# Kernel tuning notes

Measured on AMD Instinct MI355X. Metric: run time of the kernel, lower is better.

Reference implementation:

```python
import jax, jax.numpy as jnp
import numpy as np

N_TOKEN = 8192
N_EMBED = 512
N_SAMPLE = 10
TAU = 1.0
RHO = 1.0


def setup_inputs() -> dict:
    key = jax.random.key(0)
    k1, k2 = jax.random.split(key)
    inputs = jax.random.normal(k1, (4, 2048, N_EMBED), dtype=jnp.float32)
    embeds = jax.random.normal(k2, (N_TOKEN, N_EMBED), dtype=jnp.float32)
    return {"inputs": inputs, "embeds": embeds}


def reference(inputs, embeds):
    size = inputs.shape
    x = inputs.reshape(-1, N_EMBED)  # (N, D)
    n = x.shape[0]
    # squared distances, scaled by n_token (as in get_distances)
    dists = (jnp.sum(x * x, axis=-1, keepdims=True)
             + jnp.sum(embeds * embeds, axis=-1)[None, :]
             - 2.0 * jnp.matmul(x, embeds.T)) / N_TOKEN  # (N, K)
    logits = -dists / TAU  # categorical(softmax(logits)) == categorical(logits)
    skey = jax.random.fold_in(jax.random.key(0), 1)
    # multinomial with replacement: n_sample i.i.d. categorical draws per row
    samples = jax.random.categorical(skey, logits[:, None, :], axis=-1,
                                     shape=(n, N_SAMPLE))  # (N, n_sample) int
    quantized_embs = embeds[samples].mean(axis=1)  # (N, D) gather + mean
    quantized = x + jax.lax.stop_gradient(quantized_embs - x)  # straight-through
    gkey = jax.random.fold_in(jax.random.key(0), 2)
    gates = jax.random.bernoulli(gkey, RHO, (n,)).astype(x.dtype)[:, None]
    quantized = quantized * gates + (1.0 - gates) * x
    quantized = quantized.reshape(size)
    samples = samples.reshape(size[:-1] + (N_SAMPLE,))
    return quantized, samples
```

## Files before the change

### kernel.cpp

```cpp
#include <hip/hip_runtime.h>
#include <stdint.h>
#include <math.h>

#define N_ROWS 8192
#define N_TOK  8192
#define N_DIM  512
#define N_SAMP 10
#define GK     1536

typedef __attribute__((ext_vector_type(8))) short bf16x8_t;
typedef __attribute__((ext_vector_type(4))) float f32x4_t;

__host__ __device__ __forceinline__ void tf2x32(uint32_t ks0, uint32_t ks1,
                                                uint32_t& x0, uint32_t& x1) {
  uint32_t ks2 = ks0 ^ ks1 ^ 0x1BD11BDAu;
  x0 += ks0; x1 += ks1;
#define TF_ROUND(r) { x0 += x1; x1 = (x1 << (r)) | (x1 >> (32 - (r))); x1 ^= x0; }
  TF_ROUND(13) TF_ROUND(15) TF_ROUND(26) TF_ROUND(6)
  x0 += ks1; x1 += ks2 + 1u;
  TF_ROUND(17) TF_ROUND(29) TF_ROUND(16) TF_ROUND(24)
  x0 += ks2; x1 += ks0 + 2u;
  TF_ROUND(13) TF_ROUND(15) TF_ROUND(26) TF_ROUND(6)
  x0 += ks0; x1 += ks1 + 3u;
  TF_ROUND(17) TF_ROUND(29) TF_ROUND(16) TF_ROUND(24)
  x0 += ks1; x1 += ks2 + 4u;
  TF_ROUND(13) TF_ROUND(15) TF_ROUND(26) TF_ROUND(6)
  x0 += ks2; x1 += ks0 + 5u;
#undef TF_ROUND
}

__device__ __forceinline__ unsigned short f2bf_rne(float f) {
  uint32_t u = __float_as_uint(f);
  uint32_t r = (u + 0x7fffu + ((u >> 16) & 1u)) >> 16;
  return (unsigned short)r;
}
__device__ __forceinline__ float bf2f(unsigned short h) {
  return __uint_as_float((uint32_t)h << 16);
}

__device__ __forceinline__ unsigned long long shfl_xor_u64(unsigned long long v, int off) {
  uint32_t lo = (uint32_t)v, hi = (uint32_t)(v >> 32);
  lo = (uint32_t)__shfl_xor((int)lo, off, 64);
  hi = (uint32_t)__shfl_xor((int)hi, off, 64);
  return ((unsigned long long)hi << 32) | lo;
}

__global__ __launch_bounds__(256) void rownorm_kernel(const float* __restrict__ M,
                                                      float* __restrict__ out) {
  int lane = threadIdx.x & 63;
  int row = (int)((blockIdx.x * blockDim.x + threadIdx.x) >> 6);
  const float* p = M + (size_t)row * N_DIM;
  float acc = 0.f;
#pragma unroll
  for (int d = 0; d < N_DIM; d += 64) {
    float v = p[d + lane];
    acc = fmaf(v, v, acc);
  }
#pragma unroll
  for (int off = 32; off; off >>= 1) acc += __shfl_xor(acc, off, 64);
  if (lane == 0) out[row] = acc;
}

__global__ __launch_bounds__(256) void init_state_kernel(float* __restrict__ rmin,
                                                         int* __restrict__ ridx) {
  int i = blockIdx.x * 256 + threadIdx.x;
  if (i < N_ROWS * N_SAMP) { rmin[i] = INFINITY; ridx[i] = 0; }
}

__global__ __launch_bounds__(256) void split_kernel(const float* __restrict__ src,
                                                    unsigned short* __restrict__ dst,
                                                    int mode) {
  int t = blockIdx.x * 256 + threadIdx.x;
  int row = t >> 7;
  int c = (t & 127) << 2;
  float4 v = *(const float4*)(src + (size_t)row * N_DIM + c);
  ushort4 hi, lo;
  hi.x = f2bf_rne(v.x); lo.x = f2bf_rne(v.x - bf2f(hi.x));
  hi.y = f2bf_rne(v.y); lo.y = f2bf_rne(v.y - bf2f(hi.y));
  hi.z = f2bf_rne(v.z); lo.z = f2bf_rne(v.z - bf2f(hi.z));
  hi.w = f2bf_rne(v.w); lo.w = f2bf_rne(v.w - bf2f(hi.w));
  unsigned short* base = dst + (size_t)row * GK;
  *(ushort4*)(base + c) = hi;
  if (mode == 0) {
    *(ushort4*)(base + 512 + c) = lo;
    *(ushort4*)(base + 1024 + c) = hi;
  } else {
    *(ushort4*)(base + 512 + c) = hi;
    *(ushort4*)(base + 1024 + c) = lo;
  }
}

__device__ __forceinline__ void async_cp16(const void* g, void* l) {
  __builtin_amdgcn_global_load_lds((const __attribute__((address_space(1))) void*)g,
                                   (__attribute__((address_space(3))) void*)l, 16, 0, 0);
}

__global__ __launch_bounds__(256) void gemm_bf16_kernel(const unsigned short* __restrict__ A2,
                                                        const unsigned short* __restrict__ B2,
                                                        const float* __restrict__ xx,
                                                        const float* __restrict__ ee,
                                                        float* __restrict__ E,
                                                        int ks, int KC) {
  __shared__ __align__(16) unsigned short As[128 * 64];
  __shared__ __align__(16) unsigned short Bs[128 * 64];
  int tid = threadIdx.x;
  int w = tid >> 6, l = tid & 63;

  int gx = gridDim.x;
  int bid = blockIdx.y * gx + blockIdx.x;
  int band = bid / (8 * gx);
  int t8 = bid % (8 * gx);
  int by = band * 8 + (t8 & 7);
  int bx = t8 >> 3;

  int row0 = by * 128;
  int col0 = bx * 128;
  int bcol0 = ks + col0;
  int wm = (w & 1) * 64, wn = (w >> 1) * 64;
  int quad = l >> 4, r15 = l & 15;

  f32x4_t acc[4][4];
#pragma unroll
  for (int i = 0; i < 4; ++i)
#pragma unroll
    for (int j = 0; j < 4; ++j) acc[i][j] = (f32x4_t){0.f, 0.f, 0.f, 0.f};

  int srow[4], skc[4];
#pragma unroll
  for (int r = 0; r < 4; ++r) {
    int c = tid + 256 * r;
    srow[r] = c >> 3;
    skc[r] = (c & 7) ^ (srow[r] & 7);
  }

  for (int k0 = 0; k0 < GK; k0 += 64) {
#pragma unroll
    for (int r = 0; r < 4; ++r) {
      int c = tid + 256 * r;
      async_cp16(A2 + (size_t)(row0 + srow[r]) * GK + k0 + skc[r] * 8, As + c * 8);
      async_cp16(B2 + (size_t)(bcol0 + srow[r]) * GK + k0 + skc[r] * 8, Bs + c * 8);
    }
    __syncthreads();

#pragma unroll
    for (int kk2 = 0; kk2 < 2; ++kk2) {
      bf16x8_t af[4], bf[4];
#pragma unroll
      for (int i = 0; i < 4; ++i) {
        int row = wm + i * 16 + r15;
        int qc = (kk2 * 4 + quad) ^ (r15 & 7);
        af[i] = *(const bf16x8_t*)&As[row * 64 + qc * 8];
      }
#pragma unroll
      for (int j = 0; j < 4; ++j) {
        int row = wn + j * 16 + r15;
        int qc = (kk2 * 4 + quad) ^ (r15 & 7);
        bf[j] = *(const bf16x8_t*)&Bs[row * 64 + qc * 8];
      }
#pragma unroll
      for (int i = 0; i < 4; ++i)
#pragma unroll
        for (int j = 0; j < 4; ++j)
          acc[i][j] = __builtin_amdgcn_mfma_f32_16x16x32_bf16(af[i], bf[j], acc[i][j], 0, 0, 0);
    }
    __syncthreads();
  }

  const float inv_nt = 1.f / 8192.f;
  float eev[4];
#pragma unroll
  for (int j = 0; j < 4; ++j) eev[j] = ee[ks + col0 + wn + j * 16 + r15];
#pragma unroll
  for (int i = 0; i < 4; ++i) {
#pragma unroll
    for (int r = 0; r < 4; ++r) {
      int grow = row0 + wm + i * 16 + quad * 4 + r;
      float xxv = xx[grow];
#pragma unroll
      for (int j = 0; j < 4; ++j) {
        int gcol = col0 + wn + j * 16 + r15;
        float dist = (xxv + eev[j] - 2.0f * acc[i][j][r]) * inv_nt;
        E[(size_t)grow * KC + gcol] = expf(dist);
      }
    }
  }
}

__global__ __launch_bounds__(256) void gemm_nt_kernel(const float* __restrict__ A,
                                                      const float* __restrict__ B,
                                                      const float* __restrict__ xx,
                                                      const float* __restrict__ ee,
                                                      float* __restrict__ E,
                                                      int ks, int KC) {
  __shared__ __align__(16) float Asf[32][68];
  __shared__ __align__(16) float Bsf[32][68];
  int tid = threadIdx.x;
  int row0 = blockIdx.y * 64;
  int colB0 = blockIdx.x * 64 + ks;
  int tx = tid & 15, ty = tid >> 4;
  float acc[4][4] = {};
  for (int d0 = 0; d0 < N_DIM; d0 += 32) {
#pragma unroll
    for (int r = 0; r < 2; ++r) {
      int c = tid + 256 * r;
      int m = c >> 3;
      int dv = (c & 7) << 2;
      const float4 va = *(const float4*)(A + (size_t)(row0 + m) * N_DIM + d0 + dv);
      Asf[dv + 0][m] = va.x; Asf[dv + 1][m] = va.y;
      Asf[dv + 2][m] = va.z; Asf[dv + 3][m] = va.w;
      const float4 vb = *(const float4*)(B + (size_t)(colB0 + m) * N_DIM + d0 + dv);
      Bsf[dv + 0][m] = vb.x; Bsf[dv + 1][m] = vb.y;
      Bsf[dv + 2][m] = vb.z; Bsf[dv + 3][m] = vb.w;
    }
    __syncthreads();
#pragma unroll
    for (int dd = 0; dd < 32; ++dd) {
      float4 a4 = *(const float4*)&Asf[dd][ty << 2];
      float4 b4 = *(const float4*)&Bsf[dd][tx << 2];
      float av[4] = {a4.x, a4.y, a4.z, a4.w};
      float bv[4] = {b4.x, b4.y, b4.z, b4.w};
#pragma unroll
      for (int i = 0; i < 4; ++i)
#pragma unroll
        for (int j = 0; j < 4; ++j)
          acc[i][j] = fmaf(av[i], bv[j], acc[i][j]);
    }
    __syncthreads();
  }
  const float inv_nt = 1.f / 8192.f;
  int colC0 = blockIdx.x * 64;
  float eev[4];
#pragma unroll
  for (int j = 0; j < 4; ++j) eev[j] = ee[ks + colC0 + (tx << 2) + j];
#pragma unroll
  for (int i = 0; i < 4; ++i) {
    int grow = row0 + (ty << 2) + i;
    float xxv = xx[grow];
    float4 v;
    v.x = expf((xxv + eev[0] - 2.0f * acc[i][0]) * inv_nt);
    v.y = expf((xxv + eev[1] - 2.0f * acc[i][1]) * inv_nt);
    v.z = expf((xxv + eev[2] - 2.0f * acc[i][2]) * inv_nt);
    v.w = expf((xxv + eev[3] - 2.0f * acc[i][3]) * inv_nt);
    *(float4*)(E + (size_t)grow * KC + colC0 + (tx << 2)) = v;
  }
}

__global__ __launch_bounds__(256) void sample_kernel(const float* __restrict__ E,
                                                     float* __restrict__ rmin,
                                                     int* __restrict__ ridx,
                                                     int ks, int KC,
                                                     uint32_t k0, uint32_t k1) {
  int lane = threadIdx.x & 63;
  int row = (int)((blockIdx.x * blockDim.x + threadIdx.x) >> 6);
  unsigned long long champ[N_SAMP];
  uint32_t th[N_SAMP];
#pragma unroll
  for (int s = 0; s < N_SAMP; ++s) { champ[s] = 0xFFFFFFFFFFFFFFFFULL; th[s] = 0u; }
  const float tiny = 1.1754943508222875e-38f;
  uint32_t row_c = (uint32_t)row * 81920u;
  const float* Erow = E + (size_t)row * KC;

  float Ek = Erow[lane];
  for (int kk = lane; kk < KC; kk += 64) {
    int nk = (kk + 64 < KC) ? kk + 64 : kk;
    float Ekn = Erow[nk];
    uint32_t k = (uint32_t)(ks + kk);
    uint32_t base_c = row_c + k;
#pragma unroll
    for (int s = 0; s < N_SAMP; ++s) {
      uint32_t x0 = 0u, x1 = base_c + (uint32_t)s * 8192u;
      tf2x32(k0, k1, x0, x1);
      uint32_t bits = x0 ^ x1;
      bool cand = (bits >= th[s]);
      if (__any(cand)) {
        float u = __uint_as_float(0x3f800000u | (bits >> 9)) - 1.0f;
        u = fmaxf(u, tiny);
        float wv = -logf(u) * Ek;
        unsigned long long p = cand
            ? (((unsigned long long)__float_as_uint(wv) << 32) | k)
            : 0xFFFFFFFFFFFFFFFFULL;
#pragma unroll
        for (int off = 1; off < 64; off <<= 1) {
          unsigned long long op = shfl_xor_u64(p, off);
          p = (op < p) ? op : p;
        }
        if (p < champ[s]) {
          champ[s] = p;
          float wmin = __uint_as_float((uint32_t)(p >> 32));
          float ut = expf(-wmin) * 0.999999f;
          th[s] = ((uint32_t)(ut * 8388608.0f)) << 9;
        }
      }
    }
    Ek = Ekn;
  }
#pragma unroll
  for (int s = 0; s < N_SAMP; ++s) {
    if (lane == 0) {
      float v = __uint_as_float((uint32_t)(champ[s] >> 32));
      int id = (int)(uint32_t)(champ[s] & 0xFFFFFFFFu);
      size_t p = (size_t)row * N_SAMP + s;
      if (v < rmin[p]) { rmin[p] = v; ridx[p] = id; }
    }
  }
}

__global__ __launch_bounds__(256) void gather_kernel(const float* __restrict__ emb,
                                                     const int* __restrict__ ridx,
                                                     const float* __restrict__ x,
                                                     float* __restrict__ outq,
                                                     float* __restrict__ outs) {
  int lane = threadIdx.x & 63;
  int row = (int)((blockIdx.x * blockDim.x + threadIdx.x) >> 6);
  int idx[N_SAMP];
#pragma unroll
  for (int s = 0; s < N_SAMP; ++s) idx[s] = ridx[row * N_SAMP + s];
  if (lane < N_SAMP) outs[row * N_SAMP + lane] = (float)idx[lane];
#pragma unroll
  for (int h = 0; h < 2; ++h) {
    int c = h * 256 + lane * 4;
    float4 sum = make_float4(0.f, 0.f, 0.f, 0.f);
#pragma unroll
    for (int s = 0; s < N_SAMP; ++s) {
      float4 e = *(const float4*)(emb + (size_t)idx[s] * N_DIM + c);
      sum.x += e.x; sum.y += e.y; sum.z += e.z; sum.w += e.w;
    }
    float4 xv = *(const float4*)(x + (size_t)row * N_DIM + c);
    float4 o;
    o.x = xv.x + (sum.x / 10.0f - xv.x);
    o.y = xv.y + (sum.y / 10.0f - xv.y);
    o.z = xv.z + (sum.z / 10.0f - xv.z);
    o.w = xv.w + (sum.w / 10.0f - xv.w);
    *(float4*)(outq + (size_t)row * N_DIM + c) = o;
  }
}

extern "C" void kernel_launch(void* const* d_in, const int* in_sizes, int n_in,
                              void* d_out, int out_size, void* d_ws, size_t ws_size,
                              hipStream_t stream) {
  const float* x = (const float*)d_in[0];
  const float* emb = (const float*)d_in[1];
  float* out_q = (float*)d_out;
  float* out_s = out_q + (size_t)N_ROWS * N_DIM;

  const size_t fixed_f = (size_t)N_ROWS + N_TOK + 2 * (size_t)N_ROWS * N_SAMP;
  const size_t out_f = (size_t)N_ROWS * N_DIM + (size_t)N_ROWS * N_SAMP;
  const size_t split_u = (size_t)N_ROWS * GK;

  uint32_t s0 = 0u, s1 = 1u;
  tf2x32(0u, 0u, s0, s1);

  int KC = 0;
  for (int c = 8192; c >= 128; c >>= 1) {
    size_t need = fixed_f * 4 + 2 * split_u * 2 + (size_t)N_ROWS * c * 4;
    if (need <= ws_size) { KC = c; break; }
  }

  if (KC) {
    float* xx = (float*)d_ws;
    float* ee = xx + N_ROWS;
    float* rmin = ee + N_TOK;
    int* ridx = (int*)(rmin + (size_t)N_ROWS * N_SAMP);
    unsigned short* A2 = (unsigned short*)(ridx + (size_t)N_ROWS * N_SAMP);
    unsigned short* B2 = A2 + split_u;
    float* E = (float*)(B2 + split_u);

    rownorm_kernel<<<2048, 256, 0, stream>>>(x, xx);
    rownorm_kernel<<<2048, 256, 0, stream>>>(emb, ee);
    init_state_kernel<<<(N_ROWS * N_SAMP + 255) / 256, 256, 0, stream>>>(rmin, ridx);
    split_kernel<<<N_ROWS * 128 / 256, 256, 0, stream>>>(x, A2, 0);
    split_kernel<<<N_ROWS * 128 / 256, 256, 0, stream>>>(emb, B2, 1);

    for (int ks = 0; ks < N_TOK; ks += KC) {
      gemm_bf16_kernel<<<dim3(KC / 128, N_ROWS / 128), 256, 0, stream>>>(A2, B2, xx, ee, E, ks, KC);
      sample_kernel<<<2048, 256, 0, stream>>>(E, rmin, ridx, ks, KC, s0, s1);
    }
    gather_kernel<<<2048, 256, 0, stream>>>(emb, ridx, x, out_q, out_s);
    return;
  }

  float *xx, *ee, *rmin, *E;
  int* ridx;
  KC = 0;
  for (int c = 8192; c >= 64; c >>= 1) {
    if ((fixed_f + (size_t)N_ROWS * c) * 4 <= ws_size) { KC = c; break; }
  }
  if (KC) {
    xx = (float*)d_ws;
    ee = xx + N_ROWS;
    rmin = ee + N_TOK;
    ridx = (int*)(rmin + (size_t)N_ROWS * N_SAMP);
    E = (float*)(ridx + (size_t)N_ROWS * N_SAMP);
  } else if (fixed_f * 4 <= ws_size) {
    KC = 512;
    xx = (float*)d_ws;
    ee = xx + N_ROWS;
    rmin = ee + N_TOK;
    ridx = (int*)(rmin + (size_t)N_ROWS * N_SAMP);
    E = out_q;
  } else {
    KC = 256;
    E = out_q;
    float* tail = out_q + (out_f - fixed_f);
    xx = tail;
    ee = xx + N_ROWS;
    rmin = ee + N_TOK;
    ridx = (int*)(rmin + (size_t)N_ROWS * N_SAMP);
  }

  rownorm_kernel<<<2048, 256, 0, stream>>>(x, xx);
  rownorm_kernel<<<2048, 256, 0, stream>>>(emb, ee);
  init_state_kernel<<<(N_ROWS * N_SAMP + 255) / 256, 256, 0, stream>>>(rmin, ridx);
  for (int ks = 0; ks < N_TOK; ks += KC) {
    gemm_nt_kernel<<<dim3(KC / 64, N_ROWS / 64), 256, 0, stream>>>(x, emb, xx, ee, E, ks, KC);
    sample_kernel<<<2048, 256, 0, stream>>>(E, rmin, ridx, ks, KC, s0, s1);
  }
  gather_kernel<<<2048, 256, 0, stream>>>(emb, ridx, x, out_q, out_s);
}
```

Measured before the change: 1.629 ms.

## Fuse sampling into bf16 GEMM epilogue with packed 64-bit atomicMin champions

Removes the materialized exp-distance matrix E and the separate sample kernel. The GEMM epilogue now generates Threefry randoms per (row, sample, column), computes exponential-race weights and reduces them across 16 lanes. It merges the winner into a global packed (weight, index) champion with atomicMin. A per-row threshold is read from the current champion, so columns that cannot win skip the log/exp work. This trades the large E write and reread for much more ALU work per output tile (10 samples × RNG per element), plus atomic contention.

```diff
diff --git a/kernel.cpp b/kernel.cpp
--- a/kernel.cpp
+++ b/kernel.cpp
@@ -59,6 +59,11 @@
 #pragma unroll
   for (int off = 32; off; off >>= 1) acc += __shfl_xor(acc, off, 64);
   if (lane == 0) out[row] = acc;
+}
+
+__global__ __launch_bounds__(256) void init_champ_kernel(unsigned long long* __restrict__ c) {
+  int i = blockIdx.x * 256 + threadIdx.x;
+  if (i < N_ROWS * N_SAMP) c[i] = 0xFFFFFFFFFFFFFFFFULL;
 }
 
 __global__ __launch_bounds__(256) void init_state_kernel(float* __restrict__ rmin,
@@ -95,14 +100,13 @@
                                    (__attribute__((address_space(3))) void*)l, 16, 0, 0);
 }
 
-__global__ __launch_bounds__(256) void gemm_bf16_kernel(const unsigned short* __restrict__ A2,
-                                                        const unsigned short* __restrict__ B2,
-                                                        const float* __restrict__ xx,
-                                                        const float* __restrict__ ee,
-                                                        float* __restrict__ E,
-                                                        int ks, int KC) {
+__global__ __launch_bounds__(256) void fused_gemm_sample_kernel(
+    const unsigned short* __restrict__ A2, const unsigned short* __restrict__ B2,
+    const float* __restrict__ xx, const float* __restrict__ ee,
+    unsigned long long* __restrict__ champ, uint32_t k0, uint32_t k1) {
   __shared__ __align__(16) unsigned short As[128 * 64];
   __shared__ __align__(16) unsigned short Bs[128 * 64];
+  __shared__ uint32_t thr[128 * N_SAMP];
   int tid = threadIdx.x;
   int w = tid >> 6, l = tid & 63;
 
@@ -115,7 +119,6 @@
 
   int row0 = by * 128;
   int col0 = bx * 128;
-  int bcol0 = ks + col0;
   int wm = (w & 1) * 64, wn = (w >> 1) * 64;
   int quad = l >> 4, r15 = l & 15;
 
@@ -133,12 +136,12 @@
     skc[r] = (c & 7) ^ (srow[r] & 7);
   }
 
-  for (int k0 = 0; k0 < GK; k0 += 64) {
+  for (int kt = 0; kt < GK; kt += 64) {
 #pragma unroll
     for (int r = 0; r < 4; ++r) {
       int c = tid + 256 * r;
-      async_cp16(A2 + (size_t)(row0 + srow[r]) * GK + k0 + skc[r] * 8, As + c * 8);
-      async_cp16(B2 + (size_t)(bcol0 + srow[r]) * GK + k0 + skc[r] * 8, Bs + c * 8);
+      async_cp16(A2 + (size_t)(row0 + srow[r]) * GK + kt + skc[r] * 8, As + c * 8);
+      async_cp16(B2 + (size_t)(col0 + srow[r]) * GK + kt + skc[r] * 8, Bs + c * 8);
     }
     __syncthreads();
 
@@ -166,21 +169,71 @@
     __syncthreads();
   }
 
+#pragma unroll 1
+  for (int t = tid; t < 128 * N_SAMP; t += 256) {
+    int rl = t / N_SAMP;
+    int s = t - rl * N_SAMP;
+    unsigned long long c = champ[(size_t)(row0 + rl) * N_SAMP + s];
+    uint32_t hi = (uint32_t)(c >> 32);
+    uint32_t th = 0u;
+    if (hi < 0x7F800000u) {
+      float ut = expf(-__uint_as_float(hi)) * 0.999999f;
+      th = ((uint32_t)(ut * 8388608.0f)) << 9;
+    }
+    thr[t] = th;
+  }
+  __syncthreads();
+
   const float inv_nt = 1.f / 8192.f;
+  const float tiny = 1.1754943508222875e-38f;
   float eev[4];
 #pragma unroll
-  for (int j = 0; j < 4; ++j) eev[j] = ee[ks + col0 + wn + j * 16 + r15];
+  for (int j = 0; j < 4; ++j) eev[j] = ee[col0 + wn + j * 16 + r15];
+  int cb = col0 + wn + r15;
+
 #pragma unroll
   for (int i = 0; i < 4; ++i) {
 #pragma unroll
     for (int r = 0; r < 4; ++r) {
-      int grow = row0 + wm + i * 16 + quad * 4 + r;
+      int lrow = wm + i * 16 + quad * 4 + r;
+      int grow = row0 + lrow;
       float xxv = xx[grow];
-#pragma unroll
-      for (int j = 0; j < 4; ++j) {
-        int gcol = col0 + wn + j * 16 + r15;
-        float dist = (xxv + eev[j] - 2.0f * acc[i][j][r]) * inv_nt;
-        E[(size_t)grow * KC + gcol] = expf(dist);
+      float dist[4];
+#pragma unroll
+      for (int j = 0; j < 4; ++j)
+        dist[j] = (xxv + eev[j] - 2.0f * acc[i][j][r]) * inv_nt;
+      uint32_t row_c = (uint32_t)grow * 81920u;
+#pragma unroll 1
+      for (int s = 0; s < N_SAMP; ++s) {
+        uint32_t th = thr[lrow * N_SAMP + s];
+        uint32_t sb = row_c + (uint32_t)s * 8192u;
+        unsigned long long ch = 0xFFFFFFFFFFFFFFFFULL;
+#pragma unroll
+        for (int j = 0; j < 4; ++j) {
+          uint32_t kk = (uint32_t)(cb + j * 16);
+          uint32_t x0 = 0u, x1 = sb + kk;
+          tf2x32(k0, k1, x0, x1);
+          uint32_t bits = x0 ^ x1;
+          if (bits >= th) {
+            float u = __uint_as_float(0x3f800000u | (bits >> 9)) - 1.0f;
+            u = fmaxf(u, tiny);
+            float wv = -logf(u) * expf(dist[j]);
+            unsigned long long p = ((unsigned long long)__float_as_uint(wv) << 32) | kk;
+            if (p < ch) ch = p;
+          }
+        }
+        unsigned long long ball = __ballot(ch != 0xFFFFFFFFFFFFFFFFULL);
+        if ((ball >> (quad << 4)) & 0xFFFFULL) {
+#pragma unroll
+          for (int off = 1; off < 16; off <<= 1) {
+            unsigned long long op = shfl_xor_u64(ch, off);
+            if (op < ch) ch = op;
+          }
+          if (r15 == 0) {
+            unsigned long long* cp = champ + (size_t)grow * N_SAMP + s;
+            if (ch < *cp) atomicMin(cp, ch);
+          }
+        }
       }
     }
   }
@@ -306,7 +359,7 @@
 }
 
 __global__ __launch_bounds__(256) void gather_kernel(const float* __restrict__ emb,
-                                                     const int* __restrict__ ridx,
+                                                     const unsigned long long* __restrict__ champ,
                                                      const float* __restrict__ x,
                                                      float* __restrict__ outq,
                                                      float* __restrict__ outs) {
@@ -314,7 +367,8 @@
   int row = (int)((blockIdx.x * blockDim.x + threadIdx.x) >> 6);
   int idx[N_SAMP];
 #pragma unroll
-  for (int s = 0; s < N_SAMP; ++s) idx[s] = ridx[row * N_SAMP + s];
+  for (int s = 0; s < N_SAMP; ++s)
+    idx[s] = (int)(uint32_t)(champ[(size_t)row * N_SAMP + s] & 0xFFFFFFFFu);
   if (lane < N_SAMP) outs[row * N_SAMP + lane] = (float)idx[lane];
 #pragma unroll
   for (int h = 0; h < 2; ++h) {
@@ -335,6 +389,36 @@
   }
 }
 
+__global__ __launch_bounds__(256) void gather_fb_kernel(const float* __restrict__ emb,
+                                                        const int* __restrict__ ridx,
+                                                        const float* __restrict__ x,
+                                                        float* __restrict__ outq,
+                                                        float* __restrict__ outs) {
+  int lane = threadIdx.x & 63;
+  int row = (int)((blockIdx.x * blockDim.x + threadIdx.x) >> 6);
+  int idx[N_SAMP];
+#pragma unroll
+  for (int s = 0; s < N_SAMP; ++s) idx[s] = ridx[row * N_SAMP + s];
+  if (lane < N_SAMP) outs[row * N_SAMP + lane] = (float)idx[lane];
+#pragma unroll
+  for (int h = 0; h < 2; ++h) {
+    int c = h * 256 + lane * 4;
+    float4 sum = make_float4(0.f, 0.f, 0.f, 0.f);
+#pragma unroll
+    for (int s = 0; s < N_SAMP; ++s) {
+      float4 e = *(const float4*)(emb + (size_t)idx[s] * N_DIM + c);
+      sum.x += e.x; sum.y += e.y; sum.z += e.z; sum.w += e.w;
+    }
+    float4 xv = *(const float4*)(x + (size_t)row * N_DIM + c);
+    float4 o;
+    o.x = xv.x + (sum.x / 10.0f - xv.x);
+    o.y = xv.y + (sum.y / 10.0f - xv.y);
+    o.z = xv.z + (sum.z / 10.0f - xv.z);
+    o.w = xv.w + (sum.w / 10.0f - xv.w);
+    *(float4*)(outq + (size_t)row * N_DIM + c) = o;
+  }
+}
+
 extern "C" void kernel_launch(void* const* d_in, const int* in_sizes, int n_in,
                               void* d_out, int out_size, void* d_ws, size_t ws_size,
                               hipStream_t stream) {
@@ -343,45 +427,39 @@
   float* out_q = (float*)d_out;
   float* out_s = out_q + (size_t)N_ROWS * N_DIM;
 
+  const size_t split_u = (size_t)N_ROWS * GK;
   const size_t fixed_f = (size_t)N_ROWS + N_TOK + 2 * (size_t)N_ROWS * N_SAMP;
   const size_t out_f = (size_t)N_ROWS * N_DIM + (size_t)N_ROWS * N_SAMP;
-  const size_t split_u = (size_t)N_ROWS * GK;
 
   uint32_t s0 = 0u, s1 = 1u;
   tf2x32(0u, 0u, s0, s1);
 
-  int KC = 0;
-  for (int c = 8192; c >= 128; c >>= 1) {
-    size_t need = fixed_f * 4 + 2 * split_u * 2 + (size_t)N_ROWS * c * 4;
-    if (need <= ws_size) { KC = c; break; }
-  }
-
-  if (KC) {
-    float* xx = (float*)d_ws;
-    float* ee = xx + N_ROWS;
-    float* rmin = ee + N_TOK;
-    int* ridx = (int*)(rmin + (size_t)N_ROWS * N_SAMP);
-    unsigned short* A2 = (unsigned short*)(ridx + (size_t)N_ROWS * N_SAMP);
-    unsigned short* B2 = A2 + split_u;
-    float* E = (float*)(B2 + split_u);
-
-    rownorm_kernel<<<2048, 256, 0, stream>>>(x, xx);
-    rownorm_kernel<<<2048, 256, 0, stream>>>(emb, ee);
-    init_state_kernel<<<(N_ROWS * N_SAMP + 255) / 256, 256, 0, stream>>>(rmin, ridx);
-    split_kernel<<<N_ROWS * 128 / 256, 256, 0, stream>>>(x, A2, 0);
-    split_kernel<<<N_ROWS * 128 / 256, 256, 0, stream>>>(emb, B2, 1);
-
-    for (int ks = 0; ks < N_TOK; ks += KC) {
-      gemm_bf16_kernel<<<dim3(KC / 128, N_ROWS / 128), 256, 0, stream>>>(A2, B2, xx, ee, E, ks, KC);
-      sample_kernel<<<2048, 256, 0, stream>>>(E, rmin, ridx, ks, KC, s0, s1);
-    }
-    gather_kernel<<<2048, 256, 0, stream>>>(emb, ridx, x, out_q, out_s);
-    return;
+  {
+    size_t need = (size_t)(N_ROWS + N_TOK) * 4
+                + (size_t)N_ROWS * N_SAMP * 8
+                + 2 * split_u * 2;
+    if (need <= ws_size) {
+      float* xx = (float*)d_ws;
+      float* ee = xx + N_ROWS;
+      unsigned long long* champ = (unsigned long long*)(ee + N_TOK);
+      unsigned short* A2 = (unsigned short*)(champ + (size_t)N_ROWS * N_SAMP);
+      unsigned short* B2 = A2 + split_u;
+
+      rownorm_kernel<<<2048, 256, 0, stream>>>(x, xx);
+      rownorm_kernel<<<2048, 256, 0, stream>>>(emb, ee);
+      init_champ_kernel<<<(N_ROWS * N_SAMP + 255) / 256, 256, 0, stream>>>(champ);
+      split_kernel<<<N_ROWS * 128 / 256, 256, 0, stream>>>(x, A2, 0);
+      split_kernel<<<N_ROWS * 128 / 256, 256, 0, stream>>>(emb, B2, 1);
+      fused_gemm_sample_kernel<<<dim3(N_TOK / 128, N_ROWS / 128), 256, 0, stream>>>(
+          A2, B2, xx, ee, champ, s0, s1);
+      gather_kernel<<<2048, 256, 0, stream>>>(emb, champ, x, out_q, out_s);
+      return;
+    }
   }
 
   float *xx, *ee, *rmin, *E;
   int* ridx;
-  KC = 0;
+  int KC = 0;
   for (int c = 8192; c >= 64; c >>= 1) {
     if ((fixed_f + (size_t)N_ROWS * c) * 4 <= ws_size) { KC = c; break; }
   }
@@ -415,5 +493,5 @@
     gemm_nt_kernel<<<dim3(KC / 64, N_ROWS / 64), 256, 0, stream>>>(x, emb, xx, ee, E, ks, KC);
     sample_kernel<<<2048, 256, 0, stream>>>(E, rmin, ridx, ks, KC, s0, s1);
   }
-  gather_kernel<<<2048, 256, 0, stream>>>(emb, ridx, x, out_q, out_s);
-}
+  gather_fb_kernel<<<2048, 256, 0, stream>>>(emb, ridx, x, out_q, out_s);
+}
```

Result: slower. 3.982 ms (+144.5%).
